# Kernel optimization log

Hardware: AMD Instinct MI355X
Metric: run time of the kernel (lower is better)

## Reference

```python
import jax, jax.numpy as jnp
import numpy as np

N, E, G = 50000, 800000, 64
IN, HID, HEADS, OUT = 128, 64, 4, 128
NEG = 0.2  # PyG GATConv default negative_slope


def setup_inputs() -> dict:
    key = jax.random.key(0)
    ks = jax.random.split(key, 12)
    nrm = lambda k, shape, s: (jax.random.normal(k, shape, jnp.float32) * s)
    x = nrm(ks[0], (N, IN), 1.0)
    edge_index = jax.random.randint(ks[1], (2, E), 0, N)
    batch = jnp.sort(jax.random.randint(ks[2], (N,), 0, G))
    W1 = nrm(ks[3], (IN, HEADS * HID), IN ** -0.5)
    a1_src = nrm(ks[4], (HEADS, HID), HID ** -0.5)
    a1_dst = nrm(ks[5], (HEADS, HID), HID ** -0.5)
    b1 = jnp.zeros((HEADS * HID,), jnp.float32)
    W2 = nrm(ks[6], (HEADS * HID, OUT), (HEADS * HID) ** -0.5)
    a2_src = nrm(ks[7], (1, OUT), OUT ** -0.5)
    a2_dst = nrm(ks[8], (1, OUT), OUT ** -0.5)
    b2 = jnp.zeros((OUT,), jnp.float32)
    fc_W = nrm(ks[9], (OUT, OUT), OUT ** -0.5)
    fc_b = jnp.zeros((OUT,), jnp.float32)
    return dict(x=x, edge_index=edge_index, batch=batch, W1=W1, a1_src=a1_src,
                a1_dst=a1_dst, b1=b1, W2=W2, a2_src=a2_src, a2_dst=a2_dst,
                b2=b2, fc_W=fc_W, fc_b=fc_b)


def gat_conv(x, W, a_src, a_dst, b, src, dst, heads):
    n = x.shape[0]
    ch = W.shape[1] // heads
    h = (x @ W).reshape(n, heads, ch)                      # [n, H, C]
    al_s = jnp.einsum('nhc,hc->nh', h, a_src)              # per-node src logits
    al_d = jnp.einsum('nhc,hc->nh', h, a_dst)
    e = al_s[src] + al_d[dst]                              # [E, H]
    e = jnp.where(e > 0, e, NEG * e)                       # LeakyReLU
    # segment softmax over incoming edges of each dst node
    m = jax.lax.stop_gradient(jax.ops.segment_max(e, dst, num_segments=n))
    m = jnp.where(jnp.isfinite(m), m, 0.0)
    ex = jnp.exp(e - m[dst])
    s = jax.ops.segment_sum(ex, dst, num_segments=n)
    alpha = ex / (s[dst] + 1e-16)                          # [E, H]
    out = jax.ops.segment_sum(h[src] * alpha[..., None], dst, num_segments=n)
    return out.reshape(n, heads * ch) + b                  # concat heads + bias


def reference(x, edge_index, batch, W1, a1_src, a1_dst, b1, W2, a2_src, a2_dst, b2, fc_W, fc_b):
    loops = jnp.arange(N, dtype=edge_index.dtype)          # PyG adds self-loops
    src = jnp.concatenate([edge_index[0], loops])
    dst = jnp.concatenate([edge_index[1], loops])
    h = jax.nn.elu(gat_conv(x, W1, a1_src, a1_dst, b1, src, dst, HEADS))
    h = jax.nn.elu(gat_conv(h, W2, a2_src, a2_dst, b2, src, dst, 1))
    sums = jax.ops.segment_sum(h, batch, num_segments=G)
    cnt = jax.ops.segment_sum(jnp.ones((N,), h.dtype), batch, num_segments=G)
    pooled = sums / jnp.maximum(cnt, 1.0)[:, None]         # global mean pool
    return jax.nn.relu(pooled @ fc_W + fc_b)
```

## Files before the change

kernel.cpp:

```cpp
#include <hip/hip_runtime.h>
#include <math.h>

#define N_NODES 50000
#define N_EDGES 800000
#define N_GRAPHS 64
#define NEG 0.2f

typedef unsigned short us;
typedef us us2 __attribute__((ext_vector_type(2)));
typedef us us4 __attribute__((ext_vector_type(4)));
typedef us us8 __attribute__((ext_vector_type(8)));
typedef short bf16x8 __attribute__((ext_vector_type(8)));
typedef float f32x4 __attribute__((ext_vector_type(4)));

__device__ __forceinline__ us bf16rn(float f) {
  unsigned int u = __float_as_uint(f);
  u += 0x7FFFu + ((u >> 16) & 1u);
  return (us)(u >> 16);
}
__device__ __forceinline__ float bf2f(us h) {
  return __uint_as_float(((unsigned int)h) << 16);
}

__global__ __launch_bounds__(256) void convW_kernel(
    const float* __restrict__ W1, const float* __restrict__ W2,
    us* __restrict__ w1h, us* __restrict__ w1l,
    us* __restrict__ w2h, us* __restrict__ w2l) {
  int idx = blockIdx.x * 256 + threadIdx.x;
  const float* W; us *oh, *ol; int K, N, li;
  if (idx < 128 * 256) {
    W = W1; oh = w1h; ol = w1l; K = 128; N = 256; li = idx;
  } else if (idx < 2 * 128 * 256) {
    W = W2; oh = w2h; ol = w2l; K = 256; N = 128; li = idx - 128 * 256;
  } else return;
  int n = li / K, k = li - n * K;
  float f = W[(size_t)k * N + n];
  us h = bf16rn(f);
  oh[li] = h;
  ol[li] = bf16rn(f - bf2f(h));
}

__global__ __launch_bounds__(256, 2) void gemm_bf16x3(
    const float* __restrict__ A, const us* __restrict__ Bth,
    const us* __restrict__ Btl, us* __restrict__ C, int M, int N, int K) {
  __shared__ us Ah[128][40];
  __shared__ us Al[128][40];
  __shared__ us Bh[128][40];
  __shared__ us Bl[128][40];
  int t = threadIdx.x;
  int m0 = blockIdx.x * 128;
  int n0 = blockIdx.y * 128;
  int w = t >> 6, l = t & 63;
  int wr = w >> 1, wc = w & 1;
  int l15 = l & 15, g = l >> 4;

  f32x4 acc[4][4] = {};

  for (int kb = 0; kb < K; kb += 32) {
    #pragma unroll
    for (int i = 0; i < 4; i++) {
      int slot = i * 256 + t;
      int row = slot >> 3, kq = slot & 7;
      float4 v = make_float4(0.f, 0.f, 0.f, 0.f);
      if (m0 + row < M) v = *(const float4*)&A[(size_t)(m0 + row) * K + kb + kq * 4];
      us h0 = bf16rn(v.x), h1 = bf16rn(v.y), h2 = bf16rn(v.z), h3 = bf16rn(v.w);
      us4 hv = {h0, h1, h2, h3};
      us4 lv = {bf16rn(v.x - bf2f(h0)), bf16rn(v.y - bf2f(h1)),
                bf16rn(v.z - bf2f(h2)), bf16rn(v.w - bf2f(h3))};
      *(us4*)&Ah[row][kq * 4] = hv;
      *(us4*)&Al[row][kq * 4] = lv;
    }
    #pragma unroll
    for (int i = 0; i < 2; i++) {
      int slot = i * 256 + t;
      int n = slot >> 2, kq = slot & 3;
      size_t gidx = (size_t)(n0 + n) * K + kb + kq * 8;
      *(us8*)&Bh[n][kq * 8] = *(const us8*)&Bth[gidx];
      *(us8*)&Bl[n][kq * 8] = *(const us8*)&Btl[gidx];
    }
    __syncthreads();

    bf16x8 af[4], al4[4], bf[4], bl4[4];
    #pragma unroll
    for (int i = 0; i < 4; i++) {
      af[i]  = *(const bf16x8*)&Ah[wr * 64 + i * 16 + l15][g * 8];
      al4[i] = *(const bf16x8*)&Al[wr * 64 + i * 16 + l15][g * 8];
      bf[i]  = *(const bf16x8*)&Bh[wc * 64 + i * 16 + l15][g * 8];
      bl4[i] = *(const bf16x8*)&Bl[wc * 64 + i * 16 + l15][g * 8];
    }
    #pragma unroll
    for (int i = 0; i < 4; i++)
      #pragma unroll
      for (int j = 0; j < 4; j++) {
        acc[i][j] = __builtin_amdgcn_mfma_f32_16x16x32_bf16(af[i], bf[j], acc[i][j], 0, 0, 0);
        acc[i][j] = __builtin_amdgcn_mfma_f32_16x16x32_bf16(af[i], bl4[j], acc[i][j], 0, 0, 0);
        acc[i][j] = __builtin_amdgcn_mfma_f32_16x16x32_bf16(al4[i], bf[j], acc[i][j], 0, 0, 0);
      }
    __syncthreads();
  }

  #pragma unroll
  for (int i = 0; i < 4; i++)
    #pragma unroll
    for (int j = 0; j < 4; j++)
      #pragma unroll
      for (int r = 0; r < 4; r++) {
        int row = m0 + wr * 64 + i * 16 + g * 4 + r;
        if (row < M) {
          int col = n0 + wc * 64 + j * 16 + l15;
          C[(size_t)row * N + col] = bf16rn(acc[i][j][r]);
        }
      }
}

__global__ __launch_bounds__(256) void logits1_kernel(
    const us* __restrict__ h1b, const float* __restrict__ a_src,
    const float* __restrict__ a_dst, float* __restrict__ al_s,
    float* __restrict__ al_d) {
  int idx = blockIdx.x * 256 + threadIdx.x;
  if (idx >= N_NODES * 4) return;
  int n = idx >> 2, h = idx & 3;
  const us* hp = &h1b[(size_t)n * 256 + h * 64];
  float ss = 0.f, sd = 0.f;
  #pragma unroll
  for (int i = 0; i < 8; i++) {
    us8 v = *(const us8*)&hp[i * 8];
    #pragma unroll
    for (int j = 0; j < 8; j++) {
      float f = bf2f(v[j]);
      ss += f * a_src[h * 64 + i * 8 + j];
      sd += f * a_dst[h * 64 + i * 8 + j];
    }
  }
  al_s[idx] = ss;
  al_d[idx] = sd;
}

__global__ __launch_bounds__(256) void logits2_kernel(
    const us* __restrict__ h2b, const float* __restrict__ a_src,
    const float* __restrict__ a_dst, float* __restrict__ al_s,
    float* __restrict__ al_d) {
  int n = blockIdx.x * 256 + threadIdx.x;
  if (n >= N_NODES) return;
  const us* hp = &h2b[(size_t)n * 128];
  float ss = 0.f, sd = 0.f;
  #pragma unroll
  for (int i = 0; i < 16; i++) {
    us8 v = *(const us8*)&hp[i * 8];
    #pragma unroll
    for (int j = 0; j < 8; j++) {
      float f = bf2f(v[j]);
      ss += f * a_src[i * 8 + j];
      sd += f * a_dst[i * 8 + j];
    }
  }
  al_s[n] = ss;
  al_d[n] = sd;
}

__global__ __launch_bounds__(256) void count_kernel(const int* __restrict__ dst,
                                                    int* __restrict__ cnt) {
  int e = blockIdx.x * 256 + threadIdx.x;
  if (e < N_EDGES) atomicAdd(&cnt[dst[e]], 1);
}

__global__ __launch_bounds__(256) void scan1_kernel(const int* __restrict__ cnt,
                                                    int* __restrict__ itmp,
                                                    int* __restrict__ bsum) {
  int i = blockIdx.x * 256 + threadIdx.x;
  int v = (i < N_NODES) ? cnt[i] : 0;
  int lane = threadIdx.x & 63, w = threadIdx.x >> 6;
  int s = v;
  #pragma unroll
  for (int off = 1; off < 64; off <<= 1) {
    int tv = __shfl_up(s, off);
    if (lane >= off) s += tv;
  }
  __shared__ int wsum[4];
  if (lane == 63) wsum[w] = s;
  __syncthreads();
  int add = 0;
  for (int p = 0; p < w; p++) add += wsum[p];
  s += add;
  if (i < N_NODES) itmp[i] = s;
  if (threadIdx.x == 255) bsum[blockIdx.x] = s;
}

__global__ __launch_bounds__(256) void scan2_kernel(const int* __restrict__ bsum,
                                                    int* __restrict__ boff,
                                                    int nb) {
  int t = threadIdx.x;
  int v = (t < nb) ? bsum[t] : 0;
  int lane = t & 63, w = t >> 6;
  int s = v;
  #pragma unroll
  for (int off = 1; off < 64; off <<= 1) {
    int tv = __shfl_up(s, off);
    if (lane >= off) s += tv;
  }
  __shared__ int wsum[4];
  if (lane == 63) wsum[w] = s;
  __syncthreads();
  int add = 0;
  for (int p = 0; p < w; p++) add += wsum[p];
  s += add;
  if (t < nb) boff[t] = s - v;
}

__global__ __launch_bounds__(256) void scan3_kernel(const int* __restrict__ cnt,
                                                    const int* __restrict__ itmp,
                                                    const int* __restrict__ boff,
                                                    int* __restrict__ rowst,
                                                    int* __restrict__ cursor) {
  int i = blockIdx.x * 256 + threadIdx.x;
  if (i < N_NODES) {
    int excl = itmp[i] - cnt[i] + boff[i >> 8];
    rowst[i] = excl;
    cursor[i] = excl;
  }
  if (i == 0) rowst[N_NODES] = N_EDGES;
}

__global__ __launch_bounds__(256) void scatter_kernel(
    const int* __restrict__ src, const int* __restrict__ dst,
    int* __restrict__ cursor, int* __restrict__ csr_src) {
  int e = blockIdx.x * 256 + threadIdx.x;
  if (e < N_EDGES) {
    int p = atomicAdd(&cursor[dst[e]], 1);
    csr_src[p] = src[e];
  }
}

__device__ __forceinline__ void agg1_edge(int s, int head, int c0,
                                          float ald,
                                          const float* __restrict__ al_s,
                                          const us* __restrict__ h1b,
                                          float& wsum, float& a0, float& a1) {
  float al = al_s[s * 4 + head];
  us2 hv = *(const us2*)&h1b[(size_t)s * 256 + c0];
  float e = al + ald;
  e = e > 0.f ? e : NEG * e;
  float wgt = __expf(e);
  wsum += wgt;
  a0 += wgt * bf2f(hv[0]);
  a1 += wgt * bf2f(hv[1]);
}

__global__ __launch_bounds__(256) void agg1_kernel(
    const us* __restrict__ h1b, const float* __restrict__ al_s,
    const float* __restrict__ al_d, const int* __restrict__ rowst,
    const int* __restrict__ csrc, const float* __restrict__ b1,
    float* __restrict__ out) {
  int wid = (blockIdx.x * 256 + threadIdx.x) >> 6;
  int lane = threadIdx.x & 63;
  int d = wid >> 1, hf = wid & 1;
  if (d >= N_NODES) return;
  int c0 = hf * 128 + lane * 2;
  int head = c0 >> 6;
  float ald = al_d[d * 4 + head];
  float wsum = 0.f, a0 = 0.f, a1 = 0.f;
  int beg = rowst[d], end = rowst[d + 1];
  agg1_edge(d, head, c0, ald, al_s, h1b, wsum, a0, a1);
  int j = beg;
  for (; j + 3 < end; j += 4) {
    int s0 = csrc[j], s1 = csrc[j + 1], s2 = csrc[j + 2], s3 = csrc[j + 3];
    agg1_edge(s0, head, c0, ald, al_s, h1b, wsum, a0, a1);
    agg1_edge(s1, head, c0, ald, al_s, h1b, wsum, a0, a1);
    agg1_edge(s2, head, c0, ald, al_s, h1b, wsum, a0, a1);
    agg1_edge(s3, head, c0, ald, al_s, h1b, wsum, a0, a1);
  }
  for (; j < end; ++j) agg1_edge(csrc[j], head, c0, ald, al_s, h1b, wsum, a0, a1);
  float inv = 1.f / (wsum + 1e-16f);
  float2 bb = *(const float2*)&b1[c0];
  float o0 = a0 * inv + bb.x, o1 = a1 * inv + bb.y;
  o0 = o0 > 0.f ? o0 : expm1f(o0);
  o1 = o1 > 0.f ? o1 : expm1f(o1);
  *(float2*)&out[(size_t)d * 256 + c0] = make_float2(o0, o1);
}

__device__ __forceinline__ void agg2_edge(int s, int lane, float ald,
                                          const float* __restrict__ al_s,
                                          const us* __restrict__ h2b,
                                          float& wsum, float& a0, float& a1) {
  float e = al_s[s] + ald;
  e = e > 0.f ? e : NEG * e;
  float wgt = __expf(e);
  wsum += wgt;
  us2 hv = *(const us2*)&h2b[(size_t)s * 128 + lane * 2];
  a0 += wgt * bf2f(hv[0]);
  a1 += wgt * bf2f(hv[1]);
}

__global__ __launch_bounds__(256) void agg2_kernel(
    const us* __restrict__ h2b, const float* __restrict__ al_s,
    const float* __restrict__ al_d, const int* __restrict__ rowst,
    const int* __restrict__ csrc, const float* __restrict__ b2,
    float* __restrict__ out) {
  int d = (blockIdx.x * 256 + threadIdx.x) >> 6;
  int lane = threadIdx.x & 63;
  if (d >= N_NODES) return;
  float ald = al_d[d];
  float wsum = 0.f, a0 = 0.f, a1 = 0.f;
  int beg = rowst[d], end = rowst[d + 1];
  agg2_edge(d, lane, ald, al_s, h2b, wsum, a0, a1);
  int j = beg;
  for (; j + 3 < end; j += 4) {
    int s0 = csrc[j], s1 = csrc[j + 1], s2 = csrc[j + 2], s3 = csrc[j + 3];
    agg2_edge(s0, lane, ald, al_s, h2b, wsum, a0, a1);
    agg2_edge(s1, lane, ald, al_s, h2b, wsum, a0, a1);
    agg2_edge(s2, lane, ald, al_s, h2b, wsum, a0, a1);
    agg2_edge(s3, lane, ald, al_s, h2b, wsum, a0, a1);
  }
  for (; j < end; ++j) agg2_edge(csrc[j], lane, ald, al_s, h2b, wsum, a0, a1);
  float inv = 1.f / (wsum + 1e-16f);
  float2 bb = *(const float2*)&b2[lane * 2];
  float o0 = a0 * inv + bb.x, o1 = a1 * inv + bb.y;
  o0 = o0 > 0.f ? o0 : expm1f(o0);
  o1 = o1 > 0.f ? o1 : expm1f(o1);
  *(float2*)&out[(size_t)d * 128 + lane * 2] = make_float2(o0, o1);
}

#define PNPB 128
__global__ __launch_bounds__(256) void pool_kernel(const float* __restrict__ y,
                                                   const int* __restrict__ batch,
                                                   float* __restrict__ psum) {
  int t = threadIdx.x;
  int lane32 = t & 31;
  int sub = t >> 5;
  int base = blockIdx.x * PNPB + sub * (PNPB / 8);
  int nend = base + PNPB / 8;
  if (nend > N_NODES) nend = N_NODES;
  float4 acc = make_float4(0.f, 0.f, 0.f, 0.f);
  int curg = -1;
  for (int n = base; n < nend; ++n) {
    int g = batch[n];
    if (g != curg) {
      if (curg >= 0) {
        float* p = &psum[curg * 128 + lane32 * 4];
        atomicAdd(p + 0, acc.x); atomicAdd(p + 1, acc.y);
        atomicAdd(p + 2, acc.z); atomicAdd(p + 3, acc.w);
      }
      acc = make_float4(0.f, 0.f, 0.f, 0.f);
      curg = g;
    }
    float4 v = *(const float4*)&y[(size_t)n * 128 + lane32 * 4];
    acc.x += v.x; acc.y += v.y; acc.z += v.z; acc.w += v.w;
  }
  if (curg >= 0) {
    float* p = &psum[curg * 128 + lane32 * 4];
    atomicAdd(p + 0, acc.x); atomicAdd(p + 1, acc.y);
    atomicAdd(p + 2, acc.z); atomicAdd(p + 3, acc.w);
  }
}

__global__ __launch_bounds__(128) void fc_kernel(
    const float* __restrict__ psum, const int* __restrict__ batch,
    const float* __restrict__ fcW, const float* __restrict__ fcb,
    float* __restrict__ out) {
  __shared__ float pr[128];
  __shared__ int bounds[2];
  int g = blockIdx.x, c = threadIdx.x;
  if (c < 2) {
    int target = g + c;
    int lo = 0, hi = N_NODES;
    while (lo < hi) {
      int mid = (lo + hi) >> 1;
      if (batch[mid] < target) lo = mid + 1; else hi = mid;
    }
    bounds[c] = lo;
  }
  __syncthreads();
  float cnt = (float)(bounds[1] - bounds[0]);
  cnt = cnt > 1.f ? cnt : 1.f;
  pr[c] = psum[g * 128 + c] / cnt;
  __syncthreads();
  float s = fcb[c];
  #pragma unroll 8
  for (int k = 0; k < 128; k++) s += pr[k] * fcW[k * 128 + c];
  out[g * 128 + c] = fmaxf(s, 0.f);
}

extern "C" void kernel_launch(void* const* d_in, const int* in_sizes, int n_in,
                              void* d_out, int out_size, void* d_ws,
                              size_t ws_size, hipStream_t stream) {
  const float* x      = (const float*)d_in[0];
  const int*   ei     = (const int*)d_in[1];
  const int*   batch  = (const int*)d_in[2];
  const float* W1     = (const float*)d_in[3];
  const float* a1_src = (const float*)d_in[4];
  const float* a1_dst = (const float*)d_in[5];
  const float* b1     = (const float*)d_in[6];
  const float* W2     = (const float*)d_in[7];
  const float* a2_src = (const float*)d_in[8];
  const float* a2_dst = (const float*)d_in[9];
  const float* b2     = (const float*)d_in[10];
  const float* fc_W   = (const float*)d_in[11];
  const float* fc_b   = (const float*)d_in[12];
  float* out = (float*)d_out;

  const int* srcp = ei;
  const int* dstp = ei + N_EDGES;
  const int NB = (N_NODES + 255) / 256;

  float* x2   = (float*)d_ws;
  float* y    = x2 + (size_t)N_NODES * 256;
  float* al1s = y + (size_t)N_NODES * 128;
  float* al1d = al1s + N_NODES * 4;
  float* al2s = al1d + N_NODES * 4;
  float* al2d = al2s + N_NODES;
  float* psum = al2d + N_NODES;
  us* h1b  = (us*)(psum + N_GRAPHS * 128);
  us* h2b  = h1b + (size_t)N_NODES * 256;
  us* w1th = h2b + (size_t)N_NODES * 128;
  us* w1tl = w1th + 256 * 128;
  us* w2th = w1tl + 256 * 128;
  us* w2tl = w2th + 128 * 256;
  int* cnt    = (int*)(w2tl + 128 * 256);
  int* bsum   = cnt + N_NODES;
  int* boff   = bsum + 256;
  int* itmp   = boff + 256;
  int* rowst  = itmp + N_NODES;
  int* cursor = rowst + N_NODES + 8;
  int* csrc   = cursor + N_NODES;
  size_t needed = (size_t)((char*)(csrc + N_EDGES) - (char*)d_ws);
  if (ws_size < needed) return;

  hipMemsetAsync(cnt, 0, N_NODES * sizeof(int), stream);
  hipMemsetAsync(psum, 0, N_GRAPHS * 128 * sizeof(float), stream);

  count_kernel<<<(N_EDGES + 255) / 256, 256, 0, stream>>>(dstp, cnt);
  scan1_kernel<<<NB, 256, 0, stream>>>(cnt, itmp, bsum);
  scan2_kernel<<<1, 256, 0, stream>>>(bsum, boff, NB);
  scan3_kernel<<<NB, 256, 0, stream>>>(cnt, itmp, boff, rowst, cursor);
  scatter_kernel<<<(N_EDGES + 255) / 256, 256, 0, stream>>>(srcp, dstp, cursor, csrc);

  convW_kernel<<<(2 * 128 * 256 + 255) / 256, 256, 0, stream>>>(
      W1, W2, w1th, w1tl, w2th, w2tl);

  gemm_bf16x3<<<dim3(391, 2), 256, 0, stream>>>(x, w1th, w1tl, h1b, N_NODES, 256, 128);
  logits1_kernel<<<(N_NODES * 4 + 255) / 256, 256, 0, stream>>>(h1b, a1_src, a1_dst, al1s, al1d);
  agg1_kernel<<<(N_NODES * 2 * 64 + 255) / 256, 256, 0, stream>>>(h1b, al1s, al1d, rowst, csrc, b1, x2);

  gemm_bf16x3<<<dim3(391, 1), 256, 0, stream>>>(x2, w2th, w2tl, h2b, N_NODES, 128, 256);
  logits2_kernel<<<(N_NODES + 255) / 256, 256, 0, stream>>>(h2b, a2_src, a2_dst, al2s, al2d);
  agg2_kernel<<<(N_NODES + 3) / 4, 256, 0, stream>>>(h2b, al2s, al2d, rowst, csrc, b2, y);

  pool_kernel<<<(N_NODES + PNPB - 1) / PNPB, 256, 0, stream>>>(y, batch, psum);
  fc_kernel<<<N_GRAPHS, 128, 0, stream>>>(psum, batch, fc_W, fc_b, out);
}
```

Measured before the change: 337.0 us.

## Precompute per-edge attention weights in CSR order before aggregation

The scatter step now records each edge's CSR position, and two new per-edge kernels compute exp(leakyrelu(al_s+al_d)) directly into CSR-ordered weight arrays. The aggregation kernels then read these precomputed weights instead of gathering al_s and evaluating exp in every lane. This removes redundant per-lane exp and logit gathers in the inner loops. In exchange it adds two extra kernel launches, an extra int array write during scatter, and scattered writes of about 16 MB of weights.

```diff
diff --git a/kernel.cpp b/kernel.cpp
--- a/kernel.cpp
+++ b/kernel.cpp
@@ -223,24 +223,44 @@
 
 __global__ __launch_bounds__(256) void scatter_kernel(
     const int* __restrict__ src, const int* __restrict__ dst,
-    int* __restrict__ cursor, int* __restrict__ csr_src) {
+    int* __restrict__ cursor, int* __restrict__ csr_src,
+    int* __restrict__ ep) {
   int e = blockIdx.x * 256 + threadIdx.x;
   if (e < N_EDGES) {
     int p = atomicAdd(&cursor[dst[e]], 1);
     csr_src[p] = src[e];
-  }
-}
-
-__device__ __forceinline__ void agg1_edge(int s, int head, int c0,
-                                          float ald,
-                                          const float* __restrict__ al_s,
+    ep[e] = p;
+  }
+}
+
+__global__ __launch_bounds__(256) void wgt1_kernel(
+    const int* __restrict__ src, const int* __restrict__ dst,
+    const int* __restrict__ ep, const float* __restrict__ al_s,
+    const float* __restrict__ al_d, float* __restrict__ wcsr) {
+  int idx = blockIdx.x * 256 + threadIdx.x;
+  if (idx >= N_EDGES * 4) return;
+  int e = idx >> 2, h = idx & 3;
+  int s = src[e], d = dst[e];
+  float v = al_s[s * 4 + h] + al_d[d * 4 + h];
+  v = v > 0.f ? v : NEG * v;
+  wcsr[(size_t)ep[e] * 4 + h] = __expf(v);
+}
+
+__global__ __launch_bounds__(256) void wgt2_kernel(
+    const int* __restrict__ src, const int* __restrict__ dst,
+    const int* __restrict__ ep, const float* __restrict__ al_s,
+    const float* __restrict__ al_d, float* __restrict__ wcsr) {
+  int e = blockIdx.x * 256 + threadIdx.x;
+  if (e >= N_EDGES) return;
+  float v = al_s[src[e]] + al_d[dst[e]];
+  v = v > 0.f ? v : NEG * v;
+  wcsr[ep[e]] = __expf(v);
+}
+
+__device__ __forceinline__ void agg1_edge(int s, float wgt, int c0,
                                           const us* __restrict__ h1b,
                                           float& wsum, float& a0, float& a1) {
-  float al = al_s[s * 4 + head];
   us2 hv = *(const us2*)&h1b[(size_t)s * 256 + c0];
-  float e = al + ald;
-  e = e > 0.f ? e : NEG * e;
-  float wgt = __expf(e);
   wsum += wgt;
   a0 += wgt * bf2f(hv[0]);
   a1 += wgt * bf2f(hv[1]);
@@ -249,27 +269,38 @@
 __global__ __launch_bounds__(256) void agg1_kernel(
     const us* __restrict__ h1b, const float* __restrict__ al_s,
     const float* __restrict__ al_d, const int* __restrict__ rowst,
-    const int* __restrict__ csrc, const float* __restrict__ b1,
-    float* __restrict__ out) {
+    const int* __restrict__ csrc, const float* __restrict__ wcsr,
+    const float* __restrict__ b1, float* __restrict__ out) {
   int wid = (blockIdx.x * 256 + threadIdx.x) >> 6;
   int lane = threadIdx.x & 63;
   int d = wid >> 1, hf = wid & 1;
   if (d >= N_NODES) return;
   int c0 = hf * 128 + lane * 2;
   int head = c0 >> 6;
-  float ald = al_d[d * 4 + head];
+  bool hi = lane >= 32;
   float wsum = 0.f, a0 = 0.f, a1 = 0.f;
   int beg = rowst[d], end = rowst[d + 1];
-  agg1_edge(d, head, c0, ald, al_s, h1b, wsum, a0, a1);
+  {
+    float v = al_s[d * 4 + head] + al_d[d * 4 + head];
+    v = v > 0.f ? v : NEG * v;
+    agg1_edge(d, __expf(v), c0, h1b, wsum, a0, a1);
+  }
   int j = beg;
   for (; j + 3 < end; j += 4) {
     int s0 = csrc[j], s1 = csrc[j + 1], s2 = csrc[j + 2], s3 = csrc[j + 3];
-    agg1_edge(s0, head, c0, ald, al_s, h1b, wsum, a0, a1);
-    agg1_edge(s1, head, c0, ald, al_s, h1b, wsum, a0, a1);
-    agg1_edge(s2, head, c0, ald, al_s, h1b, wsum, a0, a1);
-    agg1_edge(s3, head, c0, ald, al_s, h1b, wsum, a0, a1);
-  }
-  for (; j < end; ++j) agg1_edge(csrc[j], head, c0, ald, al_s, h1b, wsum, a0, a1);
+    float2 w0 = *(const float2*)&wcsr[(size_t)j * 4 + hf * 2];
+    float2 w1 = *(const float2*)&wcsr[(size_t)(j + 1) * 4 + hf * 2];
+    float2 w2 = *(const float2*)&wcsr[(size_t)(j + 2) * 4 + hf * 2];
+    float2 w3 = *(const float2*)&wcsr[(size_t)(j + 3) * 4 + hf * 2];
+    agg1_edge(s0, hi ? w0.y : w0.x, c0, h1b, wsum, a0, a1);
+    agg1_edge(s1, hi ? w1.y : w1.x, c0, h1b, wsum, a0, a1);
+    agg1_edge(s2, hi ? w2.y : w2.x, c0, h1b, wsum, a0, a1);
+    agg1_edge(s3, hi ? w3.y : w3.x, c0, h1b, wsum, a0, a1);
+  }
+  for (; j < end; ++j) {
+    float2 w0 = *(const float2*)&wcsr[(size_t)j * 4 + hf * 2];
+    agg1_edge(csrc[j], hi ? w0.y : w0.x, c0, h1b, wsum, a0, a1);
+  }
   float inv = 1.f / (wsum + 1e-16f);
   float2 bb = *(const float2*)&b1[c0];
   float o0 = a0 * inv + bb.x, o1 = a1 * inv + bb.y;
@@ -278,15 +309,11 @@
   *(float2*)&out[(size_t)d * 256 + c0] = make_float2(o0, o1);
 }
 
-__device__ __forceinline__ void agg2_edge(int s, int lane, float ald,
-                                          const float* __restrict__ al_s,
+__device__ __forceinline__ void agg2_edge(int s, float wgt, int lane,
                                           const us* __restrict__ h2b,
                                           float& wsum, float& a0, float& a1) {
-  float e = al_s[s] + ald;
-  e = e > 0.f ? e : NEG * e;
-  float wgt = __expf(e);
+  us2 hv = *(const us2*)&h2b[(size_t)s * 128 + lane * 2];
   wsum += wgt;
-  us2 hv = *(const us2*)&h2b[(size_t)s * 128 + lane * 2];
   a0 += wgt * bf2f(hv[0]);
   a1 += wgt * bf2f(hv[1]);
 }
@@ -294,24 +321,28 @@
 __global__ __launch_bounds__(256) void agg2_kernel(
     const us* __restrict__ h2b, const float* __restrict__ al_s,
     const float* __restrict__ al_d, const int* __restrict__ rowst,
-    const int* __restrict__ csrc, const float* __restrict__ b2,
-    float* __restrict__ out) {
+    const int* __restrict__ csrc, const float* __restrict__ wcsr,
+    const float* __restrict__ b2, float* __restrict__ out) {
   int d = (blockIdx.x * 256 + threadIdx.x) >> 6;
   int lane = threadIdx.x & 63;
   if (d >= N_NODES) return;
-  float ald = al_d[d];
   float wsum = 0.f, a0 = 0.f, a1 = 0.f;
   int beg = rowst[d], end = rowst[d + 1];
-  agg2_edge(d, lane, ald, al_s, h2b, wsum, a0, a1);
+  {
+    float v = al_s[d] + al_d[d];
+    v = v > 0.f ? v : NEG * v;
+    agg2_edge(d, __expf(v), lane, h2b, wsum, a0, a1);
+  }
   int j = beg;
   for (; j + 3 < end; j += 4) {
     int s0 = csrc[j], s1 = csrc[j + 1], s2 = csrc[j + 2], s3 = csrc[j + 3];
-    agg2_edge(s0, lane, ald, al_s, h2b, wsum, a0, a1);
-    agg2_edge(s1, lane, ald, al_s, h2b, wsum, a0, a1);
-    agg2_edge(s2, lane, ald, al_s, h2b, wsum, a0, a1);
-    agg2_edge(s3, lane, ald, al_s, h2b, wsum, a0, a1);
-  }
-  for (; j < end; ++j) agg2_edge(csrc[j], lane, ald, al_s, h2b, wsum, a0, a1);
+    float w0 = wcsr[j], w1 = wcsr[j + 1], w2 = wcsr[j + 2], w3 = wcsr[j + 3];
+    agg2_edge(s0, w0, lane, h2b, wsum, a0, a1);
+    agg2_edge(s1, w1, lane, h2b, wsum, a0, a1);
+    agg2_edge(s2, w2, lane, h2b, wsum, a0, a1);
+    agg2_edge(s3, w3, lane, h2b, wsum, a0, a1);
+  }
+  for (; j < end; ++j) agg2_edge(csrc[j], wcsr[j], lane, h2b, wsum, a0, a1);
   float inv = 1.f / (wsum + 1e-16f);
   float2 bb = *(const float2*)&b2[lane * 2];
   float o0 = a0 * inv + bb.x, o1 = a1 * inv + bb.y;
@@ -402,14 +433,16 @@
   const int* dstp = ei + N_EDGES;
   const int NB = (N_NODES + 255) / 256;
 
-  float* x2   = (float*)d_ws;
-  float* y    = x2 + (size_t)N_NODES * 256;
-  float* al1s = y + (size_t)N_NODES * 128;
-  float* al1d = al1s + N_NODES * 4;
-  float* al2s = al1d + N_NODES * 4;
-  float* al2d = al2s + N_NODES;
-  float* psum = al2d + N_NODES;
-  us* h1b  = (us*)(psum + N_GRAPHS * 128);
+  float* x2    = (float*)d_ws;
+  float* y     = x2 + (size_t)N_NODES * 256;
+  float* al1s  = y + (size_t)N_NODES * 128;
+  float* al1d  = al1s + N_NODES * 4;
+  float* al2s  = al1d + N_NODES * 4;
+  float* al2d  = al2s + N_NODES;
+  float* psum  = al2d + N_NODES;
+  float* wcsr1 = psum + N_GRAPHS * 128;
+  float* wcsr2 = wcsr1 + (size_t)N_EDGES * 4;
+  us* h1b  = (us*)(wcsr2 + N_EDGES);
   us* h2b  = h1b + (size_t)N_NODES * 256;
   us* w1th = h2b + (size_t)N_NODES * 128;
   us* w1tl = w1th + 256 * 128;
@@ -421,7 +454,8 @@
   int* itmp   = boff + 256;
   int* rowst  = itmp + N_NODES;
   int* cursor = rowst + N_NODES + 8;
-  int* csrc   = cursor + N_NODES;
+  int* ep     = cursor + N_NODES;
+  int* csrc   = ep + N_EDGES;
   size_t needed = (size_t)((char*)(csrc + N_EDGES) - (char*)d_ws);
   if (ws_size < needed) return;
 
@@ -432,18 +466,21 @@
   scan1_kernel<<<NB, 256, 0, stream>>>(cnt, itmp, bsum);
   scan2_kernel<<<1, 256, 0, stream>>>(bsum, boff, NB);
   scan3_kernel<<<NB, 256, 0, stream>>>(cnt, itmp, boff, rowst, cursor);
-  scatter_kernel<<<(N_EDGES + 255) / 256, 256, 0, stream>>>(srcp, dstp, cursor, csrc);
+  scatter_kernel<<<(N_EDGES + 255) / 256, 256, 0, stream>>>(srcp, dstp, cursor, csrc, ep);
 
   convW_kernel<<<(2 * 128 * 256 + 255) / 256, 256, 0, stream>>>(
       W1, W2, w1th, w1tl, w2th, w2tl);
 
   gemm_bf16x3<<<dim3(391, 2), 256, 0, stream>>>(x, w1th, w1tl, h1b, N_NODES, 256, 128);
   logits1_kernel<<<(N_NODES * 4 + 255) / 256, 256, 0, stream>>>(h1b, a1_src, a1_dst, al1s, al1d);
-  agg1_kernel<<<(N_NODES * 2 * 64 + 255) / 256, 256, 0, stream>>>(h1b, al1s, al1d, rowst, csrc, b1, x2);
+  wgt1_kernel<<<(N_EDGES * 4 + 255) / 256, 256, 0, stream>>>(srcp, dstp, ep, al1s, al1d, wcsr1);
+  agg1_kernel<<<(N_NODES * 2 * 64 + 255) / 256, 256, 0, stream>>>(
+      h1b, al1s, al1d, rowst, csrc, wcsr1, b1, x2);
 
   gemm_bf16x3<<<dim3(391, 1), 256, 0, stream>>>(x2, w2th, w2tl, h2b, N_NODES, 128, 256);
   logits2_kernel<<<(N_NODES + 255) / 256, 256, 0, stream>>>(h2b, a2_src, a2_dst, al2s, al2d);
-  agg2_kernel<<<(N_NODES + 3) / 4, 256, 0, stream>>>(h2b, al2s, al2d, rowst, csrc, b2, y);
+  wgt2_kernel<<<(N_EDGES + 255) / 256, 256, 0, stream>>>(srcp, dstp, ep, al2s, al2d, wcsr2);
+  agg2_kernel<<<(N_NODES + 3) / 4, 256, 0, stream>>>(h2b, al2s, al2d, rowst, csrc, wcsr2, b2, y);
 
   pool_kernel<<<(N_NODES + PNPB - 1) / PNPB, 256, 0, stream>>>(y, batch, psum);
   fc_kernel<<<N_GRAPHS, 128, 0, stream>>>(psum, batch, fc_W, fc_b, out);
```

Measured after the change: 380.9 us. 1.13x slower.

## Cooperative edge-weight computation with wave shuffles in GAT aggregation kernels

Applied to the files above, without the earlier changes.

Both aggregation kernels now have each lane load one neighbour index and compute its attention weight. The indices and weights are then broadcast across the wave with shuffles, so every lane no longer redundantly loads the indices and logits and evaluates exp for every edge. Layer 1 also switches from two waves per node with 2 channels per lane to one wave per node with 4 channels per lane, loaded as us4 and written as float4. This removes redundant scalar-ish loads and transcendental work but adds shuffle overhead and halves the wave count in layer 1, which lowers parallelism available for hiding gather latency.

```diff
diff --git a/kernel.cpp b/kernel.cpp
--- a/kernel.cpp
+++ b/kernel.cpp
@@ -231,64 +231,56 @@
   }
 }
 
-__device__ __forceinline__ void agg1_edge(int s, int head, int c0,
-                                          float ald,
-                                          const float* __restrict__ al_s,
-                                          const us* __restrict__ h1b,
-                                          float& wsum, float& a0, float& a1) {
-  float al = al_s[s * 4 + head];
-  us2 hv = *(const us2*)&h1b[(size_t)s * 256 + c0];
-  float e = al + ald;
-  e = e > 0.f ? e : NEG * e;
-  float wgt = __expf(e);
-  wsum += wgt;
-  a0 += wgt * bf2f(hv[0]);
-  a1 += wgt * bf2f(hv[1]);
-}
-
 __global__ __launch_bounds__(256) void agg1_kernel(
     const us* __restrict__ h1b, const float* __restrict__ al_s,
     const float* __restrict__ al_d, const int* __restrict__ rowst,
     const int* __restrict__ csrc, const float* __restrict__ b1,
     float* __restrict__ out) {
-  int wid = (blockIdx.x * 256 + threadIdx.x) >> 6;
+  int d = (blockIdx.x * 256 + threadIdx.x) >> 6;
   int lane = threadIdx.x & 63;
-  int d = wid >> 1, hf = wid & 1;
   if (d >= N_NODES) return;
-  int c0 = hf * 128 + lane * 2;
-  int head = c0 >> 6;
+  int head = lane >> 4;
+  int c0 = lane * 4;
+  int wsel = lane & 48;
   float ald = al_d[d * 4 + head];
-  float wsum = 0.f, a0 = 0.f, a1 = 0.f;
+  float wsum = 0.f, a0 = 0.f, a1 = 0.f, a2 = 0.f, a3 = 0.f;
+  {
+    float v = al_s[d * 4 + head] + ald;
+    v = v > 0.f ? v : NEG * v;
+    float w = __expf(v);
+    us4 hv = *(const us4*)&h1b[(size_t)d * 256 + c0];
+    wsum += w;
+    a0 += w * bf2f(hv[0]); a1 += w * bf2f(hv[1]);
+    a2 += w * bf2f(hv[2]); a3 += w * bf2f(hv[3]);
+  }
   int beg = rowst[d], end = rowst[d + 1];
-  agg1_edge(d, head, c0, ald, al_s, h1b, wsum, a0, a1);
-  int j = beg;
-  for (; j + 3 < end; j += 4) {
-    int s0 = csrc[j], s1 = csrc[j + 1], s2 = csrc[j + 2], s3 = csrc[j + 3];
-    agg1_edge(s0, head, c0, ald, al_s, h1b, wsum, a0, a1);
-    agg1_edge(s1, head, c0, ald, al_s, h1b, wsum, a0, a1);
-    agg1_edge(s2, head, c0, ald, al_s, h1b, wsum, a0, a1);
-    agg1_edge(s3, head, c0, ald, al_s, h1b, wsum, a0, a1);
-  }
-  for (; j < end; ++j) agg1_edge(csrc[j], head, c0, ald, al_s, h1b, wsum, a0, a1);
+  for (int j = beg; j < end; j += 16) {
+    int m = end - j;
+    m = m < 16 ? m : 16;
+    int el = lane & 15;
+    int sv = csrc[j + (el < m ? el : 0)];
+    float v = al_s[sv * 4 + head] + ald;
+    v = v > 0.f ? v : NEG * v;
+    float wv = __expf(v);
+    #pragma unroll 4
+    for (int k = 0; k < m; ++k) {
+      int s = __shfl(sv, k);
+      float w = __shfl(wv, k + wsel);
+      us4 hv = *(const us4*)&h1b[(size_t)s * 256 + c0];
+      wsum += w;
+      a0 += w * bf2f(hv[0]); a1 += w * bf2f(hv[1]);
+      a2 += w * bf2f(hv[2]); a3 += w * bf2f(hv[3]);
+    }
+  }
   float inv = 1.f / (wsum + 1e-16f);
-  float2 bb = *(const float2*)&b1[c0];
+  float4 bb = *(const float4*)&b1[c0];
   float o0 = a0 * inv + bb.x, o1 = a1 * inv + bb.y;
+  float o2 = a2 * inv + bb.z, o3 = a3 * inv + bb.w;
   o0 = o0 > 0.f ? o0 : expm1f(o0);
   o1 = o1 > 0.f ? o1 : expm1f(o1);
-  *(float2*)&out[(size_t)d * 256 + c0] = make_float2(o0, o1);
-}
-
-__device__ __forceinline__ void agg2_edge(int s, int lane, float ald,
-                                          const float* __restrict__ al_s,
-                                          const us* __restrict__ h2b,
-                                          float& wsum, float& a0, float& a1) {
-  float e = al_s[s] + ald;
-  e = e > 0.f ? e : NEG * e;
-  float wgt = __expf(e);
-  wsum += wgt;
-  us2 hv = *(const us2*)&h2b[(size_t)s * 128 + lane * 2];
-  a0 += wgt * bf2f(hv[0]);
-  a1 += wgt * bf2f(hv[1]);
+  o2 = o2 > 0.f ? o2 : expm1f(o2);
+  o3 = o3 > 0.f ? o3 : expm1f(o3);
+  *(float4*)&out[(size_t)d * 256 + c0] = make_float4(o0, o1, o2, o3);
 }
 
 __global__ __launch_bounds__(256) void agg2_kernel(
@@ -299,25 +291,40 @@
   int d = (blockIdx.x * 256 + threadIdx.x) >> 6;
   int lane = threadIdx.x & 63;
   if (d >= N_NODES) return;
+  int c0 = lane * 2;
   float ald = al_d[d];
   float wsum = 0.f, a0 = 0.f, a1 = 0.f;
+  {
+    float v = al_s[d] + ald;
+    v = v > 0.f ? v : NEG * v;
+    float w = __expf(v);
+    us2 hv = *(const us2*)&h2b[(size_t)d * 128 + c0];
+    wsum += w;
+    a0 += w * bf2f(hv[0]); a1 += w * bf2f(hv[1]);
+  }
   int beg = rowst[d], end = rowst[d + 1];
-  agg2_edge(d, lane, ald, al_s, h2b, wsum, a0, a1);
-  int j = beg;
-  for (; j + 3 < end; j += 4) {
-    int s0 = csrc[j], s1 = csrc[j + 1], s2 = csrc[j + 2], s3 = csrc[j + 3];
-    agg2_edge(s0, lane, ald, al_s, h2b, wsum, a0, a1);
-    agg2_edge(s1, lane, ald, al_s, h2b, wsum, a0, a1);
-    agg2_edge(s2, lane, ald, al_s, h2b, wsum, a0, a1);
-    agg2_edge(s3, lane, ald, al_s, h2b, wsum, a0, a1);
-  }
-  for (; j < end; ++j) agg2_edge(csrc[j], lane, ald, al_s, h2b, wsum, a0, a1);
+  for (int j = beg; j < end; j += 64) {
+    int m = end - j;
+    m = m < 64 ? m : 64;
+    int sv = csrc[j + (lane < m ? lane : 0)];
+    float v = al_s[sv] + ald;
+    v = v > 0.f ? v : NEG * v;
+    float wv = __expf(v);
+    #pragma unroll 4
+    for (int k = 0; k < m; ++k) {
+      int s = __shfl(sv, k);
+      float w = __shfl(wv, k);
+      us2 hv = *(const us2*)&h2b[(size_t)s * 128 + c0];
+      wsum += w;
+      a0 += w * bf2f(hv[0]); a1 += w * bf2f(hv[1]);
+    }
+  }
   float inv = 1.f / (wsum + 1e-16f);
-  float2 bb = *(const float2*)&b2[lane * 2];
+  float2 bb = *(const float2*)&b2[c0];
   float o0 = a0 * inv + bb.x, o1 = a1 * inv + bb.y;
   o0 = o0 > 0.f ? o0 : expm1f(o0);
   o1 = o1 > 0.f ? o1 : expm1f(o1);
-  *(float2*)&out[(size_t)d * 128 + lane * 2] = make_float2(o0, o1);
+  *(float2*)&out[(size_t)d * 128 + c0] = make_float2(o0, o1);
 }
 
 #define PNPB 128
@@ -439,11 +446,13 @@
 
   gemm_bf16x3<<<dim3(391, 2), 256, 0, stream>>>(x, w1th, w1tl, h1b, N_NODES, 256, 128);
   logits1_kernel<<<(N_NODES * 4 + 255) / 256, 256, 0, stream>>>(h1b, a1_src, a1_dst, al1s, al1d);
-  agg1_kernel<<<(N_NODES * 2 * 64 + 255) / 256, 256, 0, stream>>>(h1b, al1s, al1d, rowst, csrc, b1, x2);
+  agg1_kernel<<<(N_NODES * 64 + 255) / 256, 256, 0, stream>>>(
+      h1b, al1s, al1d, rowst, csrc, b1, x2);
 
   gemm_bf16x3<<<dim3(391, 1), 256, 0, stream>>>(x2, w2th, w2tl, h2b, N_NODES, 128, 256);
   logits2_kernel<<<(N_NODES + 255) / 256, 256, 0, stream>>>(h2b, a2_src, a2_dst, al2s, al2d);
-  agg2_kernel<<<(N_NODES + 3) / 4, 256, 0, stream>>>(h2b, al2s, al2d, rowst, csrc, b2, y);
+  agg2_kernel<<<(N_NODES * 64 + 255) / 256, 256, 0, stream>>>(
+      h2b, al2s, al2d, rowst, csrc, b2, y);
 
   pool_kernel<<<(N_NODES + PNPB - 1) / PNPB, 256, 0, stream>>>(y, batch, psum);
   fc_kernel<<<N_GRAPHS, 128, 0, stream>>>(psum, batch, fc_W, fc_b, out);
```

After: 339.0 us. About the same (+0.6%).
